# Kernel tuning notes

Hardware: AMD Instinct MI355X
Metric: run time of the kernel (lower is better)

## Reference

```python
import jax, jax.numpy as jnp
import numpy as np

B, S, E, Q = 4, 4096, 1024, 8  # batch, seq, embed_dim, n_qubits


def setup_inputs() -> dict:
    key = jax.random.key(0)
    k1, k2, k3 = jax.random.split(key, 3)
    x = jax.random.normal(k1, (B, S, E), dtype=jnp.float32)
    W_enc = jax.random.normal(k2, (Q, E), dtype=jnp.float32) * (1.0 / np.sqrt(E))
    W_dec = jax.random.normal(k3, (E, Q), dtype=jnp.float32) * (1.0 / np.sqrt(Q))
    return {"x": x, "W_enc": W_enc, "W_dec": W_dec}


def reference(x, W_enc, W_dec):
    # encode tokens to rotation angles: [B,S,Q]
    angles = jnp.einsum('bse,qe->bsq', x, W_enc)
    c = jnp.cos(angles)
    # Analytic state-vector result of the circuit:
    #   RX(theta_i) on |0> then CNOT chain + ring closure, measure <Z_i>.
    # Heisenberg picture gives:
    #   <Z_0> = prod_{j=1..Q-1} cos(theta_j)
    #   <Z_i> = prod_{j=0..i}   cos(theta_j)   (i >= 1)
    p = jnp.cumprod(c, axis=-1)                      # prefix products
    q0 = jnp.prod(c[..., 1:], axis=-1, keepdims=True)
    q = jnp.concatenate([q0, p[..., 1:]], axis=-1)   # [B,S,Q] expvals
    # decode back to embed_dim and add residual
    return jnp.einsum('bsq,eq->bse', q, W_dec) + x
```

## Files before the change

### kernel.cpp

```cpp
#include <hip/hip_runtime.h>


#define EDIM 1024
#define QDIM 8
#define NTOK 16384
#define BLOCK 256
#define T 4
#define GRID (NTOK / T)

template<int CTRL>
__device__ __forceinline__ float dpp_add(float v) {
    int m = __builtin_amdgcn_update_dpp(0, __float_as_int(v), CTRL, 0xF, 0xF, true);
    return v + __int_as_float(m);
}

__device__ __forceinline__ float wave_sum63(float v) {
    v = dpp_add<0x111>(v);
    v = dpp_add<0x112>(v);
    v = dpp_add<0x114>(v);
    v = dpp_add<0x118>(v);
    v = dpp_add<0x142>(v);
    v = dpp_add<0x143>(v);
    return v;
}

__global__ __launch_bounds__(BLOCK)
void qattn_kernel(const float* __restrict__ x,
                  const float* __restrict__ W_enc,
                  const float* __restrict__ W_dec,
                  float* __restrict__ out)
{
    __shared__ float red[T][4][QDIM];

    const int t    = threadIdx.x;
    const int lane = t & 63;
    const int wave = t >> 6;
    const int e0   = t * 4;

    float wenc[QDIM][4];
#pragma unroll
    for (int q = 0; q < QDIM; ++q) {
        float4 w = *(const float4*)(W_enc + q * EDIM + e0);
        wenc[q][0] = w.x; wenc[q][1] = w.y; wenc[q][2] = w.z; wenc[q][3] = w.w;
    }
    float wdec[4][QDIM];
#pragma unroll
    for (int j = 0; j < 4; ++j) {
        float4 a = *(const float4*)(W_dec + (e0 + j) * QDIM);
        float4 b = *(const float4*)(W_dec + (e0 + j) * QDIM + 4);
        wdec[j][0] = a.x; wdec[j][1] = a.y; wdec[j][2] = a.z; wdec[j][3] = a.w;
        wdec[j][4] = b.x; wdec[j][5] = b.y; wdec[j][6] = b.z; wdec[j][7] = b.w;
    }

    const int tok0 = blockIdx.x * T;

    float4 xv[T];
#pragma unroll
    for (int i = 0; i < T; ++i)
        xv[i] = *(const float4*)(x + (size_t)(tok0 + i) * EDIM + e0);

    float partial[T][QDIM];
#pragma unroll
    for (int i = 0; i < T; ++i)
#pragma unroll
        for (int q = 0; q < QDIM; ++q)
            partial[i][q] = xv[i].x * wenc[q][0] + xv[i].y * wenc[q][1]
                          + xv[i].z * wenc[q][2] + xv[i].w * wenc[q][3];

#pragma unroll
    for (int i = 0; i < T; ++i)
#pragma unroll
        for (int q = 0; q < QDIM; ++q)
            partial[i][q] = wave_sum63(partial[i][q]);

    if (lane == 63) {
#pragma unroll
        for (int i = 0; i < T; ++i) {
            *(float4*)&red[i][wave][0] =
                make_float4(partial[i][0], partial[i][1], partial[i][2], partial[i][3]);
            *(float4*)&red[i][wave][4] =
                make_float4(partial[i][4], partial[i][5], partial[i][6], partial[i][7]);
        }
    }
    __syncthreads();

#pragma unroll
    for (int i = 0; i < T; ++i) {
        float4 lo = make_float4(0.f, 0.f, 0.f, 0.f);
        float4 hi = make_float4(0.f, 0.f, 0.f, 0.f);
#pragma unroll
        for (int w = 0; w < 4; ++w) {
            float4 a = *(const float4*)&red[i][w][0];
            float4 b = *(const float4*)&red[i][w][4];
            lo.x += a.x; lo.y += a.y; lo.z += a.z; lo.w += a.w;
            hi.x += b.x; hi.y += b.y; hi.z += b.z; hi.w += b.w;
        }
        float c[QDIM];
        c[0] = __cosf(lo.x); c[1] = __cosf(lo.y);
        c[2] = __cosf(lo.z); c[3] = __cosf(lo.w);
        c[4] = __cosf(hi.x); c[5] = __cosf(hi.y);
        c[6] = __cosf(hi.z); c[7] = __cosf(hi.w);

        float qv[QDIM];
        float q0 = c[1];
#pragma unroll
        for (int q = 2; q < QDIM; ++q) q0 *= c[q];
        qv[0] = q0;
        float p = c[0];
#pragma unroll
        for (int q = 1; q < QDIM; ++q) { p *= c[q]; qv[q] = p; }

        float4 o = xv[i];
#pragma unroll
        for (int q = 0; q < QDIM; ++q) {
            o.x += qv[q] * wdec[0][q];
            o.y += qv[q] * wdec[1][q];
            o.z += qv[q] * wdec[2][q];
            o.w += qv[q] * wdec[3][q];
        }
        *(float4*)(out + (size_t)(tok0 + i) * EDIM + e0) = o;
    }
}

extern "C" void kernel_launch(void* const* d_in, const int* in_sizes, int n_in,
                              void* d_out, int out_size, void* d_ws, size_t ws_size,
                              hipStream_t stream) {
    const float* x     = (const float*)d_in[0];
    const float* W_enc = (const float*)d_in[1];
    const float* W_dec = (const float*)d_in[2];
    float* out         = (float*)d_out;

    hipLaunchKernelGGL(qattn_kernel, dim3(GRID), dim3(BLOCK), 0, stream,
                       x, W_enc, W_dec, out);
}
```

Before: 34.64 us.

## Loop two token groups per block with x prefetch and packed FP32 math

Halves the grid so each block processes two groups of four tokens. The next group's x rows are prefetched while the current group is reduced and decoded, which spreads the W_enc/W_dec register loads over more tokens and overlaps loads with compute. The encode and decode dot products are rewritten with 2-wide float vectors so the compiler can emit packed FMA. A per-iteration shared buffer avoids a second barrier. The cost is higher register pressure from the prefetch buffers and fewer blocks in flight, which could cut memory-level parallelism on this bandwidth-bound kernel.

```diff
diff --git a/kernel.cpp b/kernel.cpp
--- a/kernel.cpp
+++ b/kernel.cpp
@@ -1,12 +1,15 @@
 #include <hip/hip_runtime.h>
 
+
+typedef float v2f __attribute__((ext_vector_type(2)));
 
 #define EDIM 1024
 #define QDIM 8
 #define NTOK 16384
 #define BLOCK 256
 #define T 4
-#define GRID (NTOK / T)
+#define GRID 2048
+#define ITERS (NTOK / (GRID * T))
 
 template<int CTRL>
 __device__ __forceinline__ float dpp_add(float v) {
@@ -24,101 +27,134 @@
     return v;
 }
 
-__global__ __launch_bounds__(BLOCK)
+__global__ __launch_bounds__(BLOCK, 4)
 void qattn_kernel(const float* __restrict__ x,
                   const float* __restrict__ W_enc,
                   const float* __restrict__ W_dec,
                   float* __restrict__ out)
 {
-    __shared__ float red[T][4][QDIM];
+    __shared__ float red[ITERS][T][4][QDIM];
 
     const int t    = threadIdx.x;
     const int lane = t & 63;
     const int wave = t >> 6;
     const int e0   = t * 4;
 
-    float wenc[QDIM][4];
+    v2f wenc2[QDIM][2];
 #pragma unroll
     for (int q = 0; q < QDIM; ++q) {
         float4 w = *(const float4*)(W_enc + q * EDIM + e0);
-        wenc[q][0] = w.x; wenc[q][1] = w.y; wenc[q][2] = w.z; wenc[q][3] = w.w;
+        wenc2[q][0] = (v2f){w.x, w.y};
+        wenc2[q][1] = (v2f){w.z, w.w};
     }
-    float wdec[4][QDIM];
+    v2f wdec2[4][4];
 #pragma unroll
     for (int j = 0; j < 4; ++j) {
         float4 a = *(const float4*)(W_dec + (e0 + j) * QDIM);
         float4 b = *(const float4*)(W_dec + (e0 + j) * QDIM + 4);
-        wdec[j][0] = a.x; wdec[j][1] = a.y; wdec[j][2] = a.z; wdec[j][3] = a.w;
-        wdec[j][4] = b.x; wdec[j][5] = b.y; wdec[j][6] = b.z; wdec[j][7] = b.w;
+        wdec2[j][0] = (v2f){a.x, a.y};
+        wdec2[j][1] = (v2f){a.z, a.w};
+        wdec2[j][2] = (v2f){b.x, b.y};
+        wdec2[j][3] = (v2f){b.z, b.w};
     }
 
-    const int tok0 = blockIdx.x * T;
+    const int tok0 = blockIdx.x * (T * ITERS);
 
     float4 xv[T];
 #pragma unroll
     for (int i = 0; i < T; ++i)
         xv[i] = *(const float4*)(x + (size_t)(tok0 + i) * EDIM + e0);
 
-    float partial[T][QDIM];
 #pragma unroll
-    for (int i = 0; i < T; ++i)
+    for (int it = 0; it < ITERS; ++it) {
+        float4 xn[T];
+        if (it + 1 < ITERS) {
 #pragma unroll
-        for (int q = 0; q < QDIM; ++q)
-            partial[i][q] = xv[i].x * wenc[q][0] + xv[i].y * wenc[q][1]
-                          + xv[i].z * wenc[q][2] + xv[i].w * wenc[q][3];
+            for (int i = 0; i < T; ++i)
+                xn[i] = *(const float4*)(x + (size_t)(tok0 + (it + 1) * T + i) * EDIM + e0);
+        }
+
+        float ang[T][QDIM];
+#pragma unroll
+        for (int i = 0; i < T; ++i) {
+            v2f x01 = (v2f){xv[i].x, xv[i].y};
+            v2f x23 = (v2f){xv[i].z, xv[i].w};
+#pragma unroll
+            for (int q = 0; q < QDIM; ++q) {
+                v2f acc = x01 * wenc2[q][0];
+                acc = __builtin_elementwise_fma(x23, wenc2[q][1], acc);
+                ang[i][q] = acc.x + acc.y;
+            }
+        }
 
 #pragma unroll
-    for (int i = 0; i < T; ++i)
+        for (int i = 0; i < T; ++i)
 #pragma unroll
-        for (int q = 0; q < QDIM; ++q)
-            partial[i][q] = wave_sum63(partial[i][q]);
+            for (int q = 0; q < QDIM; ++q)
+                ang[i][q] = wave_sum63(ang[i][q]);
 
-    if (lane == 63) {
+        if (lane == 63) {
+#pragma unroll
+            for (int i = 0; i < T; ++i) {
+                *(float4*)&red[it][i][wave][0] =
+                    make_float4(ang[i][0], ang[i][1], ang[i][2], ang[i][3]);
+                *(float4*)&red[it][i][wave][4] =
+                    make_float4(ang[i][4], ang[i][5], ang[i][6], ang[i][7]);
+            }
+        }
+        __syncthreads();
+
 #pragma unroll
         for (int i = 0; i < T; ++i) {
-            *(float4*)&red[i][wave][0] =
-                make_float4(partial[i][0], partial[i][1], partial[i][2], partial[i][3]);
-            *(float4*)&red[i][wave][4] =
-                make_float4(partial[i][4], partial[i][5], partial[i][6], partial[i][7]);
+            float4 lo = make_float4(0.f, 0.f, 0.f, 0.f);
+            float4 hi = make_float4(0.f, 0.f, 0.f, 0.f);
+#pragma unroll
+            for (int w = 0; w < 4; ++w) {
+                float4 a = *(const float4*)&red[it][i][w][0];
+                float4 b = *(const float4*)&red[it][i][w][4];
+                lo.x += a.x; lo.y += a.y; lo.z += a.z; lo.w += a.w;
+                hi.x += b.x; hi.y += b.y; hi.z += b.z; hi.w += b.w;
+            }
+            float c[QDIM];
+            c[0] = __cosf(lo.x); c[1] = __cosf(lo.y);
+            c[2] = __cosf(lo.z); c[3] = __cosf(lo.w);
+            c[4] = __cosf(hi.x); c[5] = __cosf(hi.y);
+            c[6] = __cosf(hi.z); c[7] = __cosf(hi.w);
+
+            float qv[QDIM];
+            float q0 = c[1];
+#pragma unroll
+            for (int q = 2; q < QDIM; ++q) q0 *= c[q];
+            qv[0] = q0;
+            float p = c[0];
+#pragma unroll
+            for (int q = 1; q < QDIM; ++q) { p *= c[q]; qv[q] = p; }
+
+            v2f qp[4];
+            qp[0] = (v2f){qv[0], qv[1]};
+            qp[1] = (v2f){qv[2], qv[3]};
+            qp[2] = (v2f){qv[4], qv[5]};
+            qp[3] = (v2f){qv[6], qv[7]};
+
+            float oacc[4];
+            oacc[0] = xv[i].x; oacc[1] = xv[i].y;
+            oacc[2] = xv[i].z; oacc[3] = xv[i].w;
+#pragma unroll
+            for (int j = 0; j < 4; ++j) {
+                v2f a = qp[0] * wdec2[j][0];
+                a = __builtin_elementwise_fma(qp[1], wdec2[j][1], a);
+                a = __builtin_elementwise_fma(qp[2], wdec2[j][2], a);
+                a = __builtin_elementwise_fma(qp[3], wdec2[j][3], a);
+                oacc[j] += a.x + a.y;
+            }
+            *(float4*)(out + (size_t)(tok0 + it * T + i) * EDIM + e0) =
+                make_float4(oacc[0], oacc[1], oacc[2], oacc[3]);
         }
-    }
-    __syncthreads();
 
+        if (it + 1 < ITERS) {
 #pragma unroll
-    for (int i = 0; i < T; ++i) {
-        float4 lo = make_float4(0.f, 0.f, 0.f, 0.f);
-        float4 hi = make_float4(0.f, 0.f, 0.f, 0.f);
-#pragma unroll
-        for (int w = 0; w < 4; ++w) {
-            float4 a = *(const float4*)&red[i][w][0];
-            float4 b = *(const float4*)&red[i][w][4];
-            lo.x += a.x; lo.y += a.y; lo.z += a.z; lo.w += a.w;
-            hi.x += b.x; hi.y += b.y; hi.z += b.z; hi.w += b.w;
+            for (int i = 0; i < T; ++i) xv[i] = xn[i];
         }
-        float c[QDIM];
-        c[0] = __cosf(lo.x); c[1] = __cosf(lo.y);
-        c[2] = __cosf(lo.z); c[3] = __cosf(lo.w);
-        c[4] = __cosf(hi.x); c[5] = __cosf(hi.y);
-        c[6] = __cosf(hi.z); c[7] = __cosf(hi.w);
-
-        float qv[QDIM];
-        float q0 = c[1];
-#pragma unroll
-        for (int q = 2; q < QDIM; ++q) q0 *= c[q];
-        qv[0] = q0;
-        float p = c[0];
-#pragma unroll
-        for (int q = 1; q < QDIM; ++q) { p *= c[q]; qv[q] = p; }
-
-        float4 o = xv[i];
-#pragma unroll
-        for (int q = 0; q < QDIM; ++q) {
-            o.x += qv[q] * wdec[0][q];
-            o.y += qv[q] * wdec[1][q];
-            o.z += qv[q] * wdec[2][q];
-            o.w += qv[q] * wdec[3][q];
-        }
-        *(float4*)(out + (size_t)(tok0 + i) * EDIM + e0) = o;
     }
 }
 
```

Result: slower. 54.46 us (+57.2%).
